# Optimization experiments

Measured on AMD Instinct MI355X. Metric: run time of the kernel, lower is better.

## Reference

```python
import jax, jax.numpy as jnp
import numpy as np

SHARPNESS = 2.0
EPS = 1e-12  # F.normalize default eps


def _l2norm_c(x):
    # L2-normalize along channel axis (axis=1), matching F.normalize(dim=1)
    n = jnp.sqrt(jnp.sum(x * x, axis=1, keepdims=True))
    return x / jnp.maximum(n, EPS)


def setup_inputs() -> dict:
    key = jax.random.key(0)
    k1, k2, k3 = jax.random.split(key, 3)
    N, C, H, W_ = 16, 256, 56, 56
    feat = jax.random.normal(k1, (N, C, H, W_), dtype=jnp.float32)
    W = jax.random.normal(k2, (C, C), dtype=jnp.float32) * 0.05  # 1x1 conv weight [out,in]
    b = jax.random.normal(k3, (C,), dtype=jnp.float32) * 0.05
    return {"feat": feat, "W": W, "b": b}


def reference(feat, W, b):
    N, C, H, W_ = feat.shape
    HW = H * W_
    # 1x1 conv == channel matmul
    feat_value = jnp.einsum('nchw,oc->nohw', feat, W) + b[None, :, None, None]
    feat_value = _l2norm_c(feat_value).reshape(N, C, HW)
    f = _l2norm_c(feat).reshape(N, C, HW)
    # correlation attention [N, HW, HW]
    attention = jnp.einsum('ncp,ncq->npq', f, f)
    attention = jnp.clip(attention, 0.0) ** SHARPNESS
    # bmm(feat_value, attention.transpose(1,2)) -> out[n,c,p] = sum_q fv[n,c,q] * att[n,p,q]
    out = jnp.einsum('ncq,npq->ncp', feat_value, attention)
    return out.reshape(N, C, H, W_)
```

## Files before the change

kernel.cpp:

```cpp
#include <hip/hip_runtime.h>

typedef unsigned short u16;
typedef unsigned int u32;
typedef __attribute__((ext_vector_type(8))) short short8;
typedef __attribute__((ext_vector_type(8))) u16 u16x8;
typedef __attribute__((ext_vector_type(2))) u32 u32x2;
typedef __attribute__((ext_vector_type(4))) u32 u32x4;
typedef __attribute__((ext_vector_type(4))) float f32x4;

#define NB 16
#define CC 256
#define HW 3136
#define NT 49

__device__ __forceinline__ u16 f2bf(float x) {
  u32 u = __float_as_uint(x);
  u += 0x7fffu + ((u >> 16) & 1u);
  return (u16)(u >> 16);
}

__device__ __forceinline__ u32 pk2(float a, float b) {
  return (u32)f2bf(a) | ((u32)f2bf(b) << 16);
}

__device__ __forceinline__ float relu2(float v) {
  v = fmaxf(v, 0.f);
  return v * v;
}

__device__ __forceinline__ f32x4 mfma16(short8 a, short8 b, f32x4 c) {
  return __builtin_amdgcn_mfma_f32_16x16x32_bf16(a, b, c, 0, 0, 0);
}

__device__ __forceinline__ void gl_lds16(const void* g, void* l) {
  __builtin_amdgcn_global_load_lds(
      (const __attribute__((address_space(1))) void*)g,
      (__attribute__((address_space(3))) void*)l, 16, 0, 0);
}

__global__ __launch_bounds__(256) void k_cvtw(const float* __restrict__ W,
                                              u16* __restrict__ Wbf) {
  int i = (blockIdx.x * 256 + threadIdx.x) * 4;
  f32x4 v = *(const f32x4*)(W + i);
  u32 lo = (u32)f2bf(v[0]) | ((u32)f2bf(v[1]) << 16);
  u32 hi = (u32)f2bf(v[2]) | ((u32)f2bf(v[3]) << 16);
  *(u32*)(Wbf + i) = lo;
  *(u32*)(Wbf + i + 2) = hi;
}

__global__ __launch_bounds__(256) void k_prep_f(const float* __restrict__ feat,
                                                u16* __restrict__ f_bf,
                                                float* __restrict__ norm_f) {
  int pt = blockIdx.x, n = blockIdx.y;
  int tid = threadIdx.x;
  __shared__ float tile[256][65];
  __shared__ float rinv[64];
  const float* src = feat + (size_t)n * CC * HW + pt * 64;
  int p = tid & 63;
  #pragma unroll 8
  for (int c = tid >> 6; c < 256; c += 4)
    tile[c][p] = src[(size_t)c * HW + p];
  __syncthreads();
  if (tid < 64) {
    float s = 0.f;
    #pragma unroll 16
    for (int c = 0; c < 256; ++c) { float v = tile[c][tid]; s += v * v; }
    float nv = fmaxf(sqrtf(s), 1e-12f);
    rinv[tid] = 1.0f / nv;
    norm_f[n * HW + pt * 64 + tid] = nv;
  }
  __syncthreads();
  u16* dst = f_bf + ((size_t)n * HW + pt * 64) * 256;
  #pragma unroll
  for (int j = 0; j < 8; ++j) {
    int chunk = j * 256 + tid;
    int pp = chunk >> 5;
    int c0 = (chunk & 31) * 8;
    float inv = rinv[pp];
    u16x8 o;
    #pragma unroll
    for (int k = 0; k < 8; ++k) o[k] = f2bf(tile[c0 + k][pp] * inv);
    *(u16x8*)(dst + pp * 256 + c0) = o;
  }
}

__global__ __launch_bounds__(256) void k_conv(const u16* __restrict__ Wbf,
                                              const float* __restrict__ bias,
                                              const u16* __restrict__ f_bf,
                                              const float* __restrict__ norm_f,
                                              u16* __restrict__ fv_bf) {
  int qt = blockIdx.x, n = blockIdx.y;
  int tid = threadIdx.x;
  int lane = tid & 63, w = tid >> 6;
  int lr = lane & 15, lg = lane >> 4;
  __shared__ __align__(16) char fq[32768];
  __shared__ float wred[4][64];
  __shared__ float sinv[64];

  const char* fsrc = (const char*)(f_bf + ((size_t)n * HW + qt * 64) * 256);
  #pragma unroll
  for (int rep = 0; rep < 8; ++rep) {
    int linear = rep * 4096 + tid * 16;
    int q = linear >> 9;
    int cb = linear & 0x1F0;
    u32x4 v = *(const u32x4*)(fsrc + q * 512 + cb);
    *(u32x4*)(fq + q * 512 + (cb ^ ((q & 7) << 4))) = v;
  }
  __syncthreads();

  f32x4 acc[4][4] = {};
  #pragma unroll
  for (int kk = 0; kk < 8; ++kk) {
    short8 bfr[4], afr[4];
    #pragma unroll
    for (int j = 0; j < 4; ++j) {
      int q = j * 16 + lr;
      bfr[j] = *(const short8*)(fq + q * 512 + ((kk * 64 + lg * 16) ^ ((q & 7) << 4)));
    }
    #pragma unroll
    for (int i = 0; i < 4; ++i) {
      int o = w * 64 + i * 16 + lr;
      afr[i] = *(const short8*)((const char*)Wbf + (size_t)o * 512 + kk * 64 + lg * 16);
    }
    #pragma unroll
    for (int i = 0; i < 4; ++i)
      #pragma unroll
      for (int j = 0; j < 4; ++j)
        acc[i][j] = mfma16(afr[i], bfr[j], acc[i][j]);
  }

  float nf[4];
  #pragma unroll
  for (int j = 0; j < 4; ++j) nf[j] = norm_f[n * HW + qt * 64 + j * 16 + lr];
  float partial[4] = {0.f, 0.f, 0.f, 0.f};
  #pragma unroll
  for (int i = 0; i < 4; ++i)
    #pragma unroll
    for (int r = 0; r < 4; ++r) {
      float bv = bias[w * 64 + i * 16 + lg * 4 + r];
      #pragma unroll
      for (int j = 0; j < 4; ++j) {
        float pre = acc[i][j][r] * nf[j] + bv;
        acc[i][j][r] = pre;
        partial[j] += pre * pre;
      }
    }
  #pragma unroll
  for (int j = 0; j < 4; ++j) {
    float v = partial[j];
    v += __shfl_xor(v, 16);
    v += __shfl_xor(v, 32);
    if (lane < 16) wred[w][j * 16 + lane] = v;
  }
  __syncthreads();
  if (tid < 64) {
    float s = wred[0][tid] + wred[1][tid] + wred[2][tid] + wred[3][tid];
    sinv[tid] = 1.0f / fmaxf(sqrtf(s), 1e-12f);
  }
  __syncthreads();
  u16* dst = fv_bf + (size_t)n * CC * HW + qt * 64;
  #pragma unroll
  for (int i = 0; i < 4; ++i)
    #pragma unroll
    for (int r = 0; r < 4; ++r) {
      int o = w * 64 + i * 16 + lg * 4 + r;
      #pragma unroll
      for (int j = 0; j < 4; ++j) {
        int q = j * 16 + lr;
        dst[(size_t)o * HW + q] = f2bf(acc[i][j][r] * sinv[q]);
      }
    }
}

__global__ __launch_bounds__(256, 2) void k_attn(const u16* __restrict__ f_bf,
                                                 const u16* __restrict__ fv_bf,
                                                 float* __restrict__ out) {
  int linear = blockIdx.y * NT + blockIdx.x;
  int vb = (linear & 7) * 98 + (linear >> 3);
  int n = vb / NT;
  int pt = vb - n * NT;

  int tid = threadIdx.x;
  int lane = tid & 63, w = tid >> 6;
  int lr = lane & 15, lg = lane >> 4;
  int wp = w & 1, wq = w >> 1;
  __shared__ __align__(16) char fqd[2][32768];
  __shared__ __align__(16) char attls[16384];

  const char* fbase = (const char*)f_bf + (size_t)n * HW * 512;
  const char* fvbase = (const char*)fv_bf + (size_t)n * CC * HW * 2;

  int so[8];
  #pragma unroll
  for (int r = 0; r < 8; ++r) {
    int q = w * 16 + r * 2 + (lane >> 5);
    int col = (lane & 31) * 16;
    so[r] = q * 512 + (col ^ ((q & 7) << 4));
  }

  short8 ap[2][8];
  #pragma unroll
  for (int fi = 0; fi < 2; ++fi) {
    int p = pt * 64 + wp * 32 + fi * 16 + lr;
    #pragma unroll
    for (int kk = 0; kk < 8; ++kk)
      ap[fi][kk] = *(const short8*)(fbase + (size_t)p * 512 + kk * 64 + lg * 16);
  }

  f32x4 oacc[4][4] = {};
  short8 av[2][4];

#define STAGE(QT) do {                                                        \
    const char* fsrc_ = fbase + (size_t)(QT) * 32768;                         \
    char* dbuf_ = (char*)fqd[(QT) & 1];                                       \
    _Pragma("unroll")                                                         \
    for (int r_ = 0; r_ < 8; ++r_)                                            \
      gl_lds16(fsrc_ + so[r_], dbuf_ + (w * 8 + r_) * 1024);                  \
  } while (0)

#define AVISSUE(QT) do {                                                      \
    _Pragma("unroll")                                                         \
    for (int kk_ = 0; kk_ < 2; ++kk_)                                         \
      _Pragma("unroll")                                                       \
      for (int fi_ = 0; fi_ < 4; ++fi_) {                                     \
        const char* pa_ = fvbase + (size_t)(w * 64 + fi_ * 16 + lr) * (HW*2)  \
                          + (QT) * 128 + kk_ * 64 + lg * 16;                  \
        asm volatile("global_load_dwordx4 %0, %1, off"                        \
                     : "=&v"(av[kk_][fi_]) : "v"(pa_) : "memory");            \
      }                                                                       \
  } while (0)

#define G1SWAP(QT) do {                                                       \
    const char* fq_ = fqd[(QT) & 1];                                          \
    char* atw_ = attls + ((QT) & 1) * 8192;                                   \
    f32x4 s_[2][2] = {};                                                      \
    __builtin_amdgcn_s_setprio(1);                                            \
    _Pragma("unroll")                                                         \
    for (int kk_ = 0; kk_ < 8; ++kk_) {                                       \
      short8 bq_[2];                                                          \
      _Pragma("unroll")                                                       \
      for (int fj_ = 0; fj_ < 2; ++fj_) {                                     \
        int q_ = wq * 32 + fj_ * 16 + lr;                                     \
        bq_[fj_] = *(const short8*)(fq_ + q_ * 512 +                          \
                     ((kk_ * 64 + lg * 16) ^ ((q_ & 7) << 4)));               \
      }                                                                       \
      s_[0][0] = mfma16(bq_[0], ap[0][kk_], s_[0][0]);                        \
      s_[0][1] = mfma16(bq_[1], ap[0][kk_], s_[0][1]);                        \
      s_[1][0] = mfma16(bq_[0], ap[1][kk_], s_[1][0]);                        \
      s_[1][1] = mfma16(bq_[1], ap[1][kk_], s_[1][1]);                        \
    }                                                                         \
    __builtin_amdgcn_s_setprio(0);                                            \
    _Pragma("unroll")                                                         \
    for (int fi_ = 0; fi_ < 2; ++fi_)                                         \
      _Pragma("unroll")                                                       \
      for (int fj_ = 0; fj_ < 2; ++fj_) {                                     \
        int p_ = wp * 32 + fi_ * 16 + lr;                                     \
        int q0_ = wq * 32 + fj_ * 16 + lg * 4;                                \
        u32x2 wv_;                                                            \
        wv_[0] = pk2(relu2(s_[fi_][fj_][0]), relu2(s_[fi_][fj_][1]));         \
        wv_[1] = pk2(relu2(s_[fi_][fj_][2]), relu2(s_[fi_][fj_][3]));         \
        *(u32x2*)(atw_ + p_ * 128 + ((q0_ * 2) ^ ((p_ & 7) << 4))) = wv_;     \
      }                                                                       \
  } while (0)

#define G2(RT) do {                                                           \
    const char* atr_ = attls + ((RT) & 1) * 8192;                             \
    __builtin_amdgcn_s_setprio(1);                                            \
    _Pragma("unroll")                                                         \
    for (int kk_ = 0; kk_ < 2; ++kk_) {                                       \
      short8 bt_[4];                                                          \
      _Pragma("unroll")                                                       \
      for (int fp_ = 0; fp_ < 4; ++fp_) {                                     \
        int p_ = fp_ * 16 + lr;                                               \
        bt_[fp_] = *(const short8*)(atr_ + p_ * 128 +                         \
                     ((kk_ * 64 + lg * 16) ^ ((p_ & 7) << 4)));               \
      }                                                                       \
      _Pragma("unroll")                                                       \
      for (int fi_ = 0; fi_ < 4; ++fi_)                                       \
        _Pragma("unroll")                                                     \
        for (int fp_ = 0; fp_ < 4; ++fp_)                                     \
          oacc[fi_][fp_] = mfma16(av[kk_][fi_], bt_[fp_], oacc[fi_][fp_]);    \
    }                                                                         \
    __builtin_amdgcn_s_setprio(0);                                            \
  } while (0)

#define SCHED0 __builtin_amdgcn_sched_barrier(0)

  STAGE(0);
  asm volatile("s_waitcnt vmcnt(0)" ::: "memory"); SCHED0;
  __builtin_amdgcn_s_barrier(); SCHED0;

  STAGE(1);
  G1SWAP(0);
  asm volatile("s_waitcnt vmcnt(0)" ::: "memory"); SCHED0;
  asm volatile("s_waitcnt lgkmcnt(0)" ::: "memory"); SCHED0;
  __builtin_amdgcn_s_barrier(); SCHED0;

  #pragma unroll 1
  for (int t = 1; t <= 48; ++t) {
    AVISSUE(t - 1);
    if (t < 48) STAGE(t + 1);
    G1SWAP(t);
    if (t < 48) {
      asm volatile("s_waitcnt vmcnt(8)" ::: "memory");
    } else {
      asm volatile("s_waitcnt vmcnt(0)" ::: "memory");
    }
    SCHED0;
    G2(t - 1);
    asm volatile("s_waitcnt vmcnt(0)" ::: "memory"); SCHED0;
    asm volatile("s_waitcnt lgkmcnt(0)" ::: "memory"); SCHED0;
    __builtin_amdgcn_s_barrier(); SCHED0;
  }

  AVISSUE(48);
  asm volatile("s_waitcnt vmcnt(0)" ::: "memory"); SCHED0;
  G2(48);

#undef SCHED0
#undef G2
#undef G1SWAP
#undef AVISSUE
#undef STAGE

  float* op = out + (size_t)n * CC * HW + pt * 64;
  #pragma unroll
  for (int fi = 0; fi < 4; ++fi)
    #pragma unroll
    for (int r = 0; r < 4; ++r) {
      int c = w * 64 + fi * 16 + lg * 4 + r;
      #pragma unroll
      for (int fp = 0; fp < 4; ++fp)
        op[(size_t)c * HW + fp * 16 + lr] = oacc[fi][fp][r];
    }
}

extern "C" void kernel_launch(void* const* d_in, const int* in_sizes, int n_in,
                              void* d_out, int out_size, void* d_ws, size_t ws_size,
                              hipStream_t stream) {
  const float* feat = (const float*)d_in[0];
  const float* W    = (const float*)d_in[1];
  const float* bias = (const float*)d_in[2];
  float* out = (float*)d_out;

  char* ws = (char*)d_ws;
  u16*   Wbf    = (u16*)ws;
  float* norm_f = (float*)(ws + 131072);
  u16*   f_bf   = (u16*)(ws + 331776);
  u16*   fv_bf  = (u16*)(ws + 26021888);

  k_cvtw<<<dim3(64), dim3(256), 0, stream>>>(W, Wbf);
  k_prep_f<<<dim3(NT, NB), dim3(256), 0, stream>>>(feat, f_bf, norm_f);
  k_conv<<<dim3(NT, NB), dim3(256), 0, stream>>>(Wbf, bias, f_bf, norm_f, fv_bf);
  k_attn<<<dim3(NT, NB), dim3(256), 0, stream>>>(f_bf, fv_bf, out);
}
```

Measured before the change: 296.9 us.

## Split Q-tile staging between LDS and direct register loads, reorder pipeline

Only half of each 64-row f tile is staged into LDS. Each wave loads its second 16-row fragment straight into registers with global loads. The main loop is reordered so the next tile's loads and the fv loads are issued after the G2 of the previous tile, with adjusted vmcnt waits. This halves LDS use for the f buffers and LDS read traffic, which may allow more occupancy or less LDS bandwidth pressure. In exchange it adds VGPR pressure, because eight short8 registers are held per wave. Tile rows are now loaded redundantly from global by the two wp waves, and the wait counts must stay correct.

```diff
diff --git a/kernel.cpp b/kernel.cpp
--- a/kernel.cpp
+++ b/kernel.cpp
@@ -184,19 +184,22 @@
   int lane = tid & 63, w = tid >> 6;
   int lr = lane & 15, lg = lane >> 4;
   int wp = w & 1, wq = w >> 1;
-  __shared__ __align__(16) char fqd[2][32768];
+  __shared__ __align__(16) char fqd[2][16384];
   __shared__ __align__(16) char attls[16384];
 
   const char* fbase = (const char*)f_bf + (size_t)n * HW * 512;
   const char* fvbase = (const char*)fv_bf + (size_t)n * CC * HW * 2;
 
-  int so[8];
-  #pragma unroll
-  for (int r = 0; r < 8; ++r) {
-    int q = w * 16 + r * 2 + (lane >> 5);
+  int so[4];
+  #pragma unroll
+  for (int r = 0; r < 4; ++r) {
+    int idx = w * 4 + r;
+    int s = idx * 2 + (lane >> 5);
+    int q = s + (s & 16);
     int col = (lane & 31) * 16;
-    so[r] = q * 512 + (col ^ ((q & 7) << 4));
-  }
+    so[r] = q * 512 + (col ^ ((s & 7) << 4));
+  }
+  int s1 = wq * 16 + lr;
 
   short8 ap[2][8];
   #pragma unroll
@@ -209,13 +212,16 @@
 
   f32x4 oacc[4][4] = {};
   short8 av[2][4];
+  short8 bq1r[8];
+
+#define SCHED0 __builtin_amdgcn_sched_barrier(0)
 
 #define STAGE(QT) do {                                                        \
     const char* fsrc_ = fbase + (size_t)(QT) * 32768;                         \
     char* dbuf_ = (char*)fqd[(QT) & 1];                                       \
     _Pragma("unroll")                                                         \
-    for (int r_ = 0; r_ < 8; ++r_)                                            \
-      gl_lds16(fsrc_ + so[r_], dbuf_ + (w * 8 + r_) * 1024);                  \
+    for (int r_ = 0; r_ < 4; ++r_)                                            \
+      gl_lds16(fsrc_ + so[r_], dbuf_ + (w * 4 + r_) * 1024);                  \
   } while (0)
 
 #define AVISSUE(QT) do {                                                      \
@@ -230,24 +236,36 @@
       }                                                                       \
   } while (0)
 
-#define G1SWAP(QT) do {                                                       \
+#define BQ1ISSUE(QT) do {                                                     \
+    _Pragma("unroll")                                                         \
+    for (int kk_ = 0; kk_ < 8; ++kk_) {                                       \
+      const char* pa_ = fbase +                                               \
+          (size_t)((QT) * 64 + wq * 32 + 16 + lr) * 512 + kk_ * 64 + lg * 16; \
+      asm volatile("global_load_dwordx4 %0, %1, off"                          \
+                   : "=&v"(bq1r[kk_]) : "v"(pa_) : "memory");                 \
+    }                                                                         \
+  } while (0)
+
+#define G1A(QT, S) do {                                                       \
     const char* fq_ = fqd[(QT) & 1];                                          \
+    __builtin_amdgcn_s_setprio(1);                                            \
+    _Pragma("unroll")                                                         \
+    for (int kk_ = 0; kk_ < 8; ++kk_) {                                       \
+      short8 bq0_ = *(const short8*)(fq_ + s1 * 512 +                         \
+                      ((kk_ * 64 + lg * 16) ^ ((s1 & 7) << 4)));              \
+      S[0][0] = mfma16(bq0_, ap[0][kk_], S[0][0]);                            \
+      S[1][0] = mfma16(bq0_, ap[1][kk_], S[1][0]);                            \
+    }                                                                         \
+    __builtin_amdgcn_s_setprio(0);                                            \
+  } while (0)
+
+#define G1B(QT, S) do {                                                       \
     char* atw_ = attls + ((QT) & 1) * 8192;                                   \
-    f32x4 s_[2][2] = {};                                                      \
     __builtin_amdgcn_s_setprio(1);                                            \
     _Pragma("unroll")                                                         \
     for (int kk_ = 0; kk_ < 8; ++kk_) {                                       \
-      short8 bq_[2];                                                          \
-      _Pragma("unroll")                                                       \
-      for (int fj_ = 0; fj_ < 2; ++fj_) {                                     \
-        int q_ = wq * 32 + fj_ * 16 + lr;                                     \
-        bq_[fj_] = *(const short8*)(fq_ + q_ * 512 +                          \
-                     ((kk_ * 64 + lg * 16) ^ ((q_ & 7) << 4)));               \
-      }                                                                       \
-      s_[0][0] = mfma16(bq_[0], ap[0][kk_], s_[0][0]);                        \
-      s_[0][1] = mfma16(bq_[1], ap[0][kk_], s_[0][1]);                        \
-      s_[1][0] = mfma16(bq_[0], ap[1][kk_], s_[1][0]);                        \
-      s_[1][1] = mfma16(bq_[1], ap[1][kk_], s_[1][1]);                        \
+      S[0][1] = mfma16(bq1r[kk_], ap[0][kk_], S[0][1]);                       \
+      S[1][1] = mfma16(bq1r[kk_], ap[1][kk_], S[1][1]);                       \
     }                                                                         \
     __builtin_amdgcn_s_setprio(0);                                            \
     _Pragma("unroll")                                                         \
@@ -257,8 +275,8 @@
         int p_ = wp * 32 + fi_ * 16 + lr;                                     \
         int q0_ = wq * 32 + fj_ * 16 + lg * 4;                                \
         u32x2 wv_;                                                            \
-        wv_[0] = pk2(relu2(s_[fi_][fj_][0]), relu2(s_[fi_][fj_][1]));         \
-        wv_[1] = pk2(relu2(s_[fi_][fj_][2]), relu2(s_[fi_][fj_][3]));         \
+        wv_[0] = pk2(relu2(S[fi_][fj_][0]), relu2(S[fi_][fj_][1]));           \
+        wv_[1] = pk2(relu2(S[fi_][fj_][2]), relu2(S[fi_][fj_][3]));           \
         *(u32x2*)(atw_ + p_ * 128 + ((q0_ * 2) ^ ((p_ & 7) << 4))) = wv_;     \
       }                                                                       \
   } while (0)
@@ -284,44 +302,53 @@
     __builtin_amdgcn_s_setprio(0);                                            \
   } while (0)
 
-#define SCHED0 __builtin_amdgcn_sched_barrier(0)
-
   STAGE(0);
+  BQ1ISSUE(0);
   asm volatile("s_waitcnt vmcnt(0)" ::: "memory"); SCHED0;
   __builtin_amdgcn_s_barrier(); SCHED0;
 
-  STAGE(1);
-  G1SWAP(0);
-  asm volatile("s_waitcnt vmcnt(0)" ::: "memory"); SCHED0;
-  asm volatile("s_waitcnt lgkmcnt(0)" ::: "memory"); SCHED0;
-  __builtin_amdgcn_s_barrier(); SCHED0;
+  {
+    f32x4 s_[2][2] = {};
+    G1A(0, s_);
+    G1B(0, s_);
+    STAGE(1);
+    AVISSUE(0);
+    BQ1ISSUE(1);
+    asm volatile("s_waitcnt vmcnt(16)" ::: "memory"); SCHED0;
+    asm volatile("s_waitcnt lgkmcnt(0)" ::: "memory"); SCHED0;
+    __builtin_amdgcn_s_barrier(); SCHED0;
+  }
 
   #pragma unroll 1
   for (int t = 1; t <= 48; ++t) {
-    AVISSUE(t - 1);
+    f32x4 s_[2][2] = {};
+    G1A(t, s_);
+    asm volatile("s_waitcnt vmcnt(0)" ::: "memory"); SCHED0;
+    G1B(t, s_);
     if (t < 48) STAGE(t + 1);
-    G1SWAP(t);
+    G2(t - 1);
+    AVISSUE(t);
+    if (t < 48) BQ1ISSUE(t + 1);
     if (t < 48) {
+      asm volatile("s_waitcnt vmcnt(16)" ::: "memory");
+    } else {
       asm volatile("s_waitcnt vmcnt(8)" ::: "memory");
-    } else {
-      asm volatile("s_waitcnt vmcnt(0)" ::: "memory");
     }
     SCHED0;
-    G2(t - 1);
-    asm volatile("s_waitcnt vmcnt(0)" ::: "memory"); SCHED0;
     asm volatile("s_waitcnt lgkmcnt(0)" ::: "memory"); SCHED0;
     __builtin_amdgcn_s_barrier(); SCHED0;
   }
 
-  AVISSUE(48);
   asm volatile("s_waitcnt vmcnt(0)" ::: "memory"); SCHED0;
   G2(48);
 
-#undef SCHED0
 #undef G2
-#undef G1SWAP
+#undef G1B
+#undef G1A
+#undef BQ1ISSUE
 #undef AVISSUE
 #undef STAGE
+#undef SCHED0
 
   float* op = out + (size_t)n * CC * HW + pt * 64;
   #pragma unroll
```

New measurement: 439.8 us. +48.1%, slower.
